# Kernel optimization log

Hardware: AMD Instinct MI355X
Metric: run time of the kernel (lower is better)

Reference implementation:

```python
import jax, jax.numpy as jnp
import numpy as np

B, C, H, W, D = 4, 64, 64, 64, 4
CQ = C // 8  # query/key channels


def setup_inputs() -> dict:
    key = jax.random.key(0)
    ks = jax.random.split(key, 10)
    x2d = jax.random.normal(ks[0], (B, C, H, W, D), dtype=jnp.float32)
    x3d = jax.random.normal(ks[1], (B, C, H, W, D), dtype=jnp.float32)
    # 1x1 Conv3d weights collapsed to (out_ch, in_ch) matrices + biases
    Wq = jax.random.normal(ks[2], (CQ, C), dtype=jnp.float32) * 0.05
    bq = jax.random.normal(ks[3], (CQ,), dtype=jnp.float32) * 0.05
    Wk = jax.random.normal(ks[4], (CQ, C), dtype=jnp.float32) * 0.05
    bk = jax.random.normal(ks[5], (CQ,), dtype=jnp.float32) * 0.05
    Wv = jax.random.normal(ks[6], (C, C), dtype=jnp.float32) * 0.05
    bv = jax.random.normal(ks[7], (C,), dtype=jnp.float32) * 0.05
    gamma = jax.random.normal(ks[8], (1,), dtype=jnp.float32)
    return {"x2d": x2d, "x3d": x3d, "Wq": Wq, "bq": bq, "Wk": Wk,
            "bk": bk, "Wv": Wv, "bv": bv, "gamma": gamma}


def _conv1x1(Wmat, bias, x):
    # x: (B, C, D, H, W); 1x1x1 Conv3d == channel matmul
    y = jnp.einsum('oc,bcdhw->bodhw', Wmat, x)
    return y + bias[None, :, None, None, None]


def reference(x2d, x3d, Wq, bq, Wk, bk, Wv, bv, gamma):
    x = jnp.transpose(x2d, (0, 1, 4, 2, 3))  # (B, C, D, H, W)
    b, c, d, h, w = x.shape
    n = h * w
    q = _conv1x1(Wq, bq, x).reshape(b, -1, n)   # (B, CQ*D, N)
    k = _conv1x1(Wk, bk, x).reshape(b, -1, n)   # (B, CQ*D, N)
    v = _conv1x1(Wv, bv, x).reshape(b, -1, n)   # (B, C*D, N)
    energy = jnp.einsum('bkn,bkm->bnm', q, k)   # (B, N, N), no scaling (faithful)
    attn = jax.nn.softmax(energy, axis=-1)
    # out[b,c,i] = sum_j attn[b,i,j] * v[b,c,j]
    out = jnp.einsum('bcm,bnm->bcn', v, attn)
    out = out.reshape(b, c, d, h, w)
    out = jnp.transpose(out, (0, 1, 3, 4, 2))   # back to (B, C, H, W, D)
    return gamma * out + x3d
```

## Files before the change

kernel.cpp:

```cpp
#include <hip/hip_runtime.h>
#include <hip/hip_bf16.h>

#define CH 64
#define NN 4096
#define SS 16384

typedef __attribute__((ext_vector_type(8))) short bf16x8;
typedef __attribute__((ext_vector_type(4))) float f32x4;

#define QB_OFF 0
#define KB_OFF 524288
#define VT_OFF 1048576

static __device__ __forceinline__ ushort bfbits(float x) {
    __hip_bfloat16 h = __float2bfloat16(x);
    return *(ushort*)&h;
}

static __device__ __forceinline__ void gld_lds16(const ushort* g, ushort* l) {
    __builtin_amdgcn_global_load_lds(
        (const __attribute__((address_space(1))) void*)g,
        (__attribute__((address_space(3))) void*)l, 16, 0, 0);
}

__global__ __launch_bounds__(256) void qkv_kernel(
    const float* __restrict__ x,
    const float* __restrict__ Wq, const float* __restrict__ bq,
    const float* __restrict__ Wk, const float* __restrict__ bk,
    const float* __restrict__ Wv, const float* __restrict__ bv,
    ushort* __restrict__ qb, ushort* __restrict__ kb, ushort* __restrict__ vt)
{
    __shared__ __align__(16) ushort Tqk[128 * 40];
    __shared__ __align__(16) ushort Tv[80 * 144];

    const int blk = blockIdx.x;
    const int b = blk >> 7, sup = (blk >> 2) & 31, og = blk & 3;
    const int tid = threadIdx.x;
    const int nl = tid >> 2, d = tid & 3;

    const int vcnt = (og < 2) ? 12 : 20;
    const int vo0 = (og == 0) ? 0 : (og == 1) ? 12 : (og == 2) ? 24 : 44;

    const float* xb = x + (size_t)b * CH * SS + sup * 512;

    for (int t = 0; t < 2; ++t) {
        const float* xp = xb + t * 256 + tid;
        float xr[CH];
#pragma unroll
        for (int c = 0; c < CH; ++c) xr[c] = xp[(size_t)c * SS];

        const int slot = 32 * (nl >> 4) + 8 * ((nl >> 2) & 3) + 4 * t + (nl & 3);

        if (og < 2) {
            const float* Wqk = (og == 0) ? Wq : Wk;
            const float* bqk = (og == 0) ? bq : bk;
            ushort* trow = &Tqk[(t * 64 + nl) * 40 + d];
#pragma unroll
            for (int o = 0; o < 8; o += 2) {
                float a0 = bqk[o], a1 = bqk[o + 1];
#pragma unroll
                for (int c = 0; c < CH; ++c) {
                    a0 = fmaf(Wqk[o * CH + c],       xr[c], a0);
                    a1 = fmaf(Wqk[(o + 1) * CH + c], xr[c], a1);
                }
                trow[o * 4]       = bfbits(a0);
                trow[(o + 1) * 4] = bfbits(a1);
            }
        }
        ushort* vcol = &Tv[d * 144 + slot];
        const float* Wvb = Wv + vo0 * CH;
        const float* bvb = bv + vo0;
        if (og < 2) {
#pragma unroll
            for (int j = 0; j < 12; j += 2) {
                float a0 = bvb[j], a1 = bvb[j + 1];
#pragma unroll
                for (int c = 0; c < CH; ++c) {
                    a0 = fmaf(Wvb[j * CH + c],       xr[c], a0);
                    a1 = fmaf(Wvb[(j + 1) * CH + c], xr[c], a1);
                }
                vcol[(j * 4) * 144]       = bfbits(a0);
                vcol[((j + 1) * 4) * 144] = bfbits(a1);
            }
        } else {
#pragma unroll
            for (int j = 0; j < 20; j += 2) {
                float a0 = bvb[j], a1 = bvb[j + 1];
#pragma unroll
                for (int c = 0; c < CH; ++c) {
                    a0 = fmaf(Wvb[j * CH + c],       xr[c], a0);
                    a1 = fmaf(Wvb[(j + 1) * CH + c], xr[c], a1);
                }
                vcol[(j * 4) * 144]       = bfbits(a0);
                vcol[((j + 1) * 4) * 144] = bfbits(a1);
            }
        }
    }
    __syncthreads();

    if (og < 2) {
        ushort* dst = (og == 0 ? qb : kb);
#pragma unroll
        for (int jj = 0; jj < 2; ++jj) {
            int idx = jj * 256 + tid;
            int row = idx >> 2, seg = idx & 3;
            *(uint4*)(dst + ((size_t)(b * NN + sup * 128 + row)) * 32 + seg * 8)
                = *(const uint4*)&Tqk[row * 40 + seg * 8];
        }
    }
    const int nchunks = vcnt * 64;
    ushort* vout = vt + ((size_t)((b * 32 + sup) * 256 + vo0 * 4)) * 144;
#pragma unroll
    for (int j = 0; j < 5; ++j) {
        int idx = j * 256 + tid;
        if (idx < nchunks) {
            int row = idx >> 4, seg = idx & 15;
            *(uint4*)(vout + (size_t)row * 144 + seg * 8)
                = *(const uint4*)&Tv[row * 144 + seg * 8];
        }
    }
}

__global__ __launch_bounds__(256, 2) void flash_kernel(
    const ushort* __restrict__ qb, const ushort* __restrict__ kb,
    const ushort* __restrict__ vt, const float* __restrict__ x3d,
    const float* __restrict__ gptr, float* __restrict__ out)
{
    __shared__ __align__(16) ushort Vls[2][128 * 144];
    __shared__ float lbuf[4 * 4 * 16];

    const int tid = threadIdx.x;
    const int b   = blockIdx.x >> 7;
    const int rem = blockIdx.x & 127;
    const int r0  = (rem >> 1) << 6;
    const int cvh = rem & 1;
    const int w = tid >> 6, lane = tid & 63, q = lane >> 4, l15 = lane & 15;

    bf16x8 Qf[4];
#pragma unroll
    for (int rt = 0; rt < 4; ++rt)
        Qf[rt] = *(const bf16x8*)(qb + (size_t)(b * NN + r0 + 16 * rt + l15) * 32 + 8 * q);

    f32x4 acc[8][4];
#pragma unroll
    for (int i = 0; i < 8; ++i)
#pragma unroll
        for (int j = 0; j < 4; ++j) acc[i][j] = (f32x4){0.f, 0.f, 0.f, 0.f};
    float l_acc[4] = {0.f, 0.f, 0.f, 0.f};

    const ushort* kgl = kb + (size_t)b * NN * 32 + (16 * w + l15) * 32 + 8 * q;

    const ushort* vgl = vt + ((size_t)(b * 32) * 256 + 128 * cvh) * 144;

#pragma unroll
    for (int i = 0; i < 9; ++i)
        gld_lds16(vgl + (size_t)(i * 256 + tid) * 8,
                  (ushort*)Vls[0] + (i * 256 + tid) * 8);

    bf16x8 Kn0 = *(const bf16x8*)(kgl);
    bf16x8 Kn1 = *(const bf16x8*)(kgl + 2048);

    for (int pt = 0; pt < 32; ++pt) {
        __syncthreads();
        if (pt < 31) {
            const ushort* src = vgl + (size_t)(pt + 1) * 36864;
            ushort* dst = (ushort*)Vls[(pt + 1) & 1];
#pragma unroll
            for (int i = 0; i < 9; ++i)
                gld_lds16(src + (size_t)(i * 256 + tid) * 8, dst + (i * 256 + tid) * 8);
        }
        bf16x8 Ka0 = Kn0, Ka1 = Kn1;
        if (pt < 31) {
            Kn0 = *(const bf16x8*)(kgl + (size_t)(2 * pt + 2) * 2048);
            Kn1 = *(const bf16x8*)(kgl + (size_t)(2 * pt + 3) * 2048);
        }

        f32x4 S0[4], S1[4];
#pragma unroll
        for (int rt = 0; rt < 4; ++rt)
            S0[rt] = __builtin_amdgcn_mfma_f32_16x16x32_bf16(
                Ka0, Qf[rt], (f32x4){0.f, 0.f, 0.f, 0.f}, 0, 0, 0);
#pragma unroll
        for (int rt = 0; rt < 4; ++rt)
            S1[rt] = __builtin_amdgcn_mfma_f32_16x16x32_bf16(
                Ka1, Qf[rt], (f32x4){0.f, 0.f, 0.f, 0.f}, 0, 0, 0);

        bf16x8 Pb[4];
#pragma unroll
        for (int rt = 0; rt < 4; ++rt) {
            float e0 = __expf(S0[rt][0]), e1 = __expf(S0[rt][1]);
            float e2 = __expf(S0[rt][2]), e3 = __expf(S0[rt][3]);
            float f0 = __expf(S1[rt][0]), f1 = __expf(S1[rt][1]);
            float f2 = __expf(S1[rt][2]), f3 = __expf(S1[rt][3]);
            l_acc[rt] += ((e0 + e1) + (e2 + e3)) + ((f0 + f1) + (f2 + f3));
            bf16x8 p;
            p[0] = (short)bfbits(e0); p[1] = (short)bfbits(e1);
            p[2] = (short)bfbits(e2); p[3] = (short)bfbits(e3);
            p[4] = (short)bfbits(f0); p[5] = (short)bfbits(f1);
            p[6] = (short)bfbits(f2); p[7] = (short)bfbits(f3);
            Pb[rt] = p;
        }

        const ushort* vb = Vls[pt & 1] + 32 * w + 8 * q;
#pragma unroll
        for (int cvt = 0; cvt < 8; ++cvt) {
            bf16x8 Va = *(const bf16x8*)(vb + (16 * cvt + l15) * 144);
#pragma unroll
            for (int rt = 0; rt < 4; ++rt)
                acc[cvt][rt] = __builtin_amdgcn_mfma_f32_16x16x32_bf16(
                    Va, Pb[rt], acc[cvt][rt], 0, 0, 0);
        }
    }

#pragma unroll
    for (int rt = 0; rt < 4; ++rt) {
        float v = l_acc[rt];
        v += __shfl_xor(v, 16);
        v += __shfl_xor(v, 32);
        if (lane < 16) lbuf[(w * 4 + rt) * 16 + lane] = v;
    }
    __syncthreads();
    const float linv = 1.f / (lbuf[(0 + w) * 16 + l15] + lbuf[(4 + w) * 16 + l15] +
                              lbuf[(8 + w) * 16 + l15] + lbuf[(12 + w) * 16 + l15]);
    const float gl = gptr[0] * linv;

    f32x4* Obuf = (f32x4*)&Vls[0][0];
#pragma unroll
    for (int cvt = 0; cvt < 8; ++cvt) {
        __syncthreads();
#pragma unroll
        for (int rt = 0; rt < 4; ++rt)
            Obuf[(w * 64 + lane) * 5 + rt] = acc[cvt][rt];
        __syncthreads();
        f32x4 o = Obuf[lane * 5 + w];
        o += Obuf[(64 + lane) * 5 + w];
        o += Obuf[(128 + lane) * 5 + w];
        o += Obuf[(192 + lane) * 5 + w];
        size_t addr = ((size_t)(b * CH + 32 * cvh + 4 * cvt + q) * NN
                       + (r0 + 16 * w + l15)) * 4;
        float4 xr = *(const float4*)(x3d + addr);
        float4 res;
        res.x = fmaf(gl, o[0], xr.x);
        res.y = fmaf(gl, o[1], xr.y);
        res.z = fmaf(gl, o[2], xr.z);
        res.w = fmaf(gl, o[3], xr.w);
        *(float4*)(out + addr) = res;
    }
}

extern "C" void kernel_launch(void* const* d_in, const int* in_sizes, int n_in,
                              void* d_out, int out_size, void* d_ws, size_t ws_size,
                              hipStream_t stream)
{
    const float* x2d = (const float*)d_in[0];
    const float* x3d = (const float*)d_in[1];
    const float* Wq  = (const float*)d_in[2];
    const float* bq  = (const float*)d_in[3];
    const float* Wk  = (const float*)d_in[4];
    const float* bk  = (const float*)d_in[5];
    const float* Wv  = (const float*)d_in[6];
    const float* bv  = (const float*)d_in[7];
    const float* gma = (const float*)d_in[8];

    ushort* wsb = (ushort*)d_ws;

    qkv_kernel<<<512, 256, 0, stream>>>(x2d, Wq, bq, Wk, bk, Wv, bv,
                                        wsb + QB_OFF, wsb + KB_OFF, wsb + VT_OFF);
    flash_kernel<<<512, 256, 0, stream>>>(wsb + QB_OFF, wsb + KB_OFF, wsb + VT_OFF,
                                          x3d, gma, (float*)d_out);
}
```

Measured before the change: 167.5 us.

## Fold log2e into Q projection, use exp2, and remap blocks across XCDs

The Q projection output is pre-scaled by log2(e) so the softmax numerator can use a native exp2 instead of __expf, which saves one multiply per score element in the hot loop. Both kernels also remap block indices so that blocks sharing a batch (and, in the flash kernel, the same V half) land on the same XCD under round-robin dispatch, aiming for better L2 reuse of K/V. Scaling Q before bf16 rounding slightly changes numerics.

```diff
diff --git a/kernel.cpp b/kernel.cpp
--- a/kernel.cpp
+++ b/kernel.cpp
@@ -15,6 +15,14 @@
 static __device__ __forceinline__ ushort bfbits(float x) {
     __hip_bfloat16 h = __float2bfloat16(x);
     return *(ushort*)&h;
+}
+
+static __device__ __forceinline__ float fexp2(float x) {
+#if __has_builtin(__builtin_amdgcn_exp2f)
+    return __builtin_amdgcn_exp2f(x);
+#else
+    return exp2f(x);
+#endif
 }
 
 static __device__ __forceinline__ void gld_lds16(const ushort* g, ushort* l) {
@@ -34,12 +42,17 @@
     __shared__ __align__(16) ushort Tv[80 * 144];
 
     const int blk = blockIdx.x;
-    const int b = blk >> 7, sup = (blk >> 2) & 31, og = blk & 3;
+    const int xcd = blk & 7, jb = blk >> 3;
+    const int b = xcd >> 1;
+    const int sup = ((xcd & 1) << 4) | (jb & 15);
+    const int og = jb >> 4;
     const int tid = threadIdx.x;
     const int nl = tid >> 2, d = tid & 3;
 
     const int vcnt = (og < 2) ? 12 : 20;
     const int vo0 = (og == 0) ? 0 : (og == 1) ? 12 : (og == 2) ? 24 : 44;
+
+    const float qscale = (og == 0) ? 1.4426950408889634f : 1.0f;
 
     const float* xb = x + (size_t)b * CH * SS + sup * 512;
 
@@ -63,8 +76,8 @@
                     a0 = fmaf(Wqk[o * CH + c],       xr[c], a0);
                     a1 = fmaf(Wqk[(o + 1) * CH + c], xr[c], a1);
                 }
-                trow[o * 4]       = bfbits(a0);
-                trow[(o + 1) * 4] = bfbits(a1);
+                trow[o * 4]       = bfbits(a0 * qscale);
+                trow[(o + 1) * 4] = bfbits(a1 * qscale);
             }
         }
         ushort* vcol = &Tv[d * 144 + slot];
@@ -130,10 +143,10 @@
     __shared__ float lbuf[4 * 4 * 16];
 
     const int tid = threadIdx.x;
-    const int b   = blockIdx.x >> 7;
-    const int rem = blockIdx.x & 127;
-    const int r0  = (rem >> 1) << 6;
-    const int cvh = rem & 1;
+    const int xcd = blockIdx.x & 7, jb = blockIdx.x >> 3;
+    const int b   = xcd >> 1;
+    const int r0  = (jb & 63) << 6;
+    const int cvh = xcd & 1;
     const int w = tid >> 6, lane = tid & 63, q = lane >> 4, l15 = lane & 15;
 
     bf16x8 Qf[4];
@@ -188,10 +201,10 @@
         bf16x8 Pb[4];
 #pragma unroll
         for (int rt = 0; rt < 4; ++rt) {
-            float e0 = __expf(S0[rt][0]), e1 = __expf(S0[rt][1]);
-            float e2 = __expf(S0[rt][2]), e3 = __expf(S0[rt][3]);
-            float f0 = __expf(S1[rt][0]), f1 = __expf(S1[rt][1]);
-            float f2 = __expf(S1[rt][2]), f3 = __expf(S1[rt][3]);
+            float e0 = fexp2(S0[rt][0]), e1 = fexp2(S0[rt][1]);
+            float e2 = fexp2(S0[rt][2]), e3 = fexp2(S0[rt][3]);
+            float f0 = fexp2(S1[rt][0]), f1 = fexp2(S1[rt][1]);
+            float f2 = fexp2(S1[rt][2]), f3 = fexp2(S1[rt][3]);
             l_acc[rt] += ((e0 + e1) + (e2 + e3)) + ((f0 + f1) + (f2 + f3));
             bf16x8 p;
             p[0] = (short)bfbits(e0); p[1] = (short)bfbits(e1);
```

Result: no change. 166.0 us (-0.9%).
